# Performance work log

Hardware: AMD Instinct MI355X
Metric: run time of the kernel (lower is better)

Reference implementation:

```python
import jax, jax.numpy as jnp
import numpy as np

N = 50000
E = 800000
IN_DIM = 256
HID = 128
HALF = HID // 2
OUT_DIM = 2


def setup_inputs() -> dict:
    key = jax.random.key(0)
    ks = jax.random.split(key, 16)
    s = lambda fan_in: 1.0 / np.sqrt(fan_in)
    inp = {
        "x": jax.random.normal(ks[0], (N, IN_DIM), dtype=jnp.float32),
        "edge_index": jax.random.randint(ks[1], (2, E), 0, N, dtype=jnp.int64),
        # lin_in: input_dim -> hidden
        "W_in": jax.random.uniform(ks[2], (IN_DIM, HID), jnp.float32, -s(IN_DIM), s(IN_DIM)),
        "b_in": jnp.zeros((HID,), jnp.float32),
        # lin_nor / lin_abnor: half -> hidden
        "W_nor": jax.random.uniform(ks[3], (HALF, HID), jnp.float32, -s(HALF), s(HALF)),
        "b_nor": jnp.zeros((HID,), jnp.float32),
        "W_abnor": jax.random.uniform(ks[4], (HALF, HID), jnp.float32, -s(HALF), s(HALF)),
        "b_abnor": jnp.zeros((HID,), jnp.float32),
        # attention gate
        "W_att": jax.random.uniform(ks[5], (HID, HID), jnp.float32, -s(HID), s(HID)),
        "b_att": jnp.zeros((HID,), jnp.float32),
        "v_att": jax.random.uniform(ks[6], (HID, 1), jnp.float32, -s(HID), s(HID)),
        # update linear
        "W_upd": jax.random.uniform(ks[7], (HID, HID), jnp.float32, -s(HID), s(HID)),
        "b_upd": jnp.zeros((HID,), jnp.float32),
        # classifier
        "W_cls": jax.random.uniform(ks[8], (HID, OUT_DIM), jnp.float32, -s(HID), s(HID)),
        "b_cls": jnp.zeros((OUT_DIM,), jnp.float32),
    }
    return inp


def reference(x, edge_index, W_in, b_in, W_nor, b_nor, W_abnor, b_abnor,
              W_att, b_att, v_att, W_upd, b_upd, W_cls, b_cls):
    n = x.shape[0]
    # add self loops (add_self_loops)
    loops = jnp.tile(jnp.arange(n, dtype=edge_index.dtype), (2, 1))
    ei = jnp.concatenate([edge_index, loops], axis=1)
    row, col = ei[0], ei[1]  # row = source j, col = target i

    # lin_in + leaky_relu (dropout p=0 / eval)
    h = jax.nn.leaky_relu(x @ W_in + b_in)

    # split halves and project
    x_nor = h[:, :HALF] @ W_nor + b_nor      # [N, HID]
    x_abnor = h[:, HALF:] @ W_abnor + b_abnor

    # symmetric normalization by target degree
    deg = jax.ops.segment_sum(jnp.ones_like(col, dtype=h.dtype), col, num_segments=n)
    dinv = jnp.where(deg > 0, jax.lax.rsqrt(jnp.where(deg > 0, deg, 1.0)), 0.0)
    norm = dinv[row] * dinv[col]             # [E']

    # per-edge gather
    xn_j = x_nor[row]                        # [E', HID]
    xa_j = x_abnor[row]

    # denoising attention gate: sigmoid(v^T tanh(W(xn+xa)+b))
    h_att = jnp.tanh((xn_j + xa_j) @ W_att + b_att)
    alpha = jax.nn.sigmoid(h_att @ v_att)    # [E', 1]

    msg = norm[:, None] * (alpha * xn_j + (1.0 - alpha) * xa_j)

    # scatter-add to targets
    aggr = jax.ops.segment_sum(msg, col, num_segments=n)  # [N, HID]

    upd = aggr @ W_upd + b_upd
    out = jax.nn.leaky_relu(upd) @ W_cls + b_cls
    return out
```

## Files before the change

### kernel.cpp

```cpp
#include <hip/hip_runtime.h>

#define N_NODES 50000
#define E_EDGES 800000
#define IN_DIM  256
#define HID     128
#define HALF    64
#define OUT_DIM 2
#define NW      32
#define SLOPE   0.01f

#define ST      132
#define WSLICE  (NW * ST)

#define SSTRIDE 520
#define PLANE   (8 * SSTRIDE)

#define SCAN_B  512
#define SCAN_NB ((N_NODES + SCAN_B - 1) / SCAN_B)

typedef unsigned int uint32;
typedef __attribute__((ext_vector_type(8)))  __bf16 bf16x8v;
typedef __attribute__((ext_vector_type(16))) float  f32x16;

union BF8 { bf16x8v v; unsigned short s[8]; uint4 q; };

#define FI_F 0
#define FN_F 4096
#define FA_F 5120
#define FT_F 6144
#define FU_F 8192
#define F_TOTAL 10240

__device__ __forceinline__ uint32 rne16u(uint32 u) {
    return (u + 0x7fffu + ((u >> 16) & 1u)) >> 16;
}

__device__ __forceinline__ uint32 pack_hl(float v) {
    uint32 uu = __float_as_uint(v);
    uint32 hh = rne16u(uu);
    float  fh = __uint_as_float(hh << 16);
    float  r  = v - fh;
    uint32 ll = rne16u(__float_as_uint(r));
    return (hh << 16) | ll;
}

__device__ __forceinline__ void mfma3(f32x16& acc, bf16x8v ah, bf16x8v al,
                                      bf16x8v bh, bf16x8v bl) {
    acc = __builtin_amdgcn_mfma_f32_32x32x16_bf16(ah, bh, acc, 0, 0, 0);
    acc = __builtin_amdgcn_mfma_f32_32x32x16_bf16(ah, bl, acc, 0, 0, 0);
    acc = __builtin_amdgcn_mfma_f32_32x32x16_bf16(al, bh, acc, 0, 0, 0);
}

__device__ __forceinline__ void stage_split4(__bf16* __restrict__ Ahi,
                                             __bf16* __restrict__ Alo,
                                             int rr, int k, float4 v) {
    int s_idx = k >> 4, jb = k & 7, lt = rr + 32 * ((k >> 3) & 1);
    int base = s_idx * SSTRIDE + lt * 8 + jb;
    float f[4] = {v.x, v.y, v.z, v.w};
    uint32 h[4], lo[4];
    #pragma unroll
    for (int j = 0; j < 4; j++) {
        uint32 uu = __float_as_uint(f[j]);
        uint32 hh = rne16u(uu);
        float  fh = __uint_as_float(hh << 16);
        float  r  = f[j] - fh;
        h[j] = hh; lo[j] = rne16u(__float_as_uint(r));
    }
    *(uint2*)(Ahi + base) = make_uint2(h[0] | (h[1] << 16), h[2] | (h[3] << 16));
    *(uint2*)(Alo + base) = make_uint2(lo[0] | (lo[1] << 16), lo[2] | (lo[3] << 16));
}

__device__ __forceinline__ void mfma_gemm1_pre(f32x16& acc,
        const __bf16* __restrict__ Ahi, const __bf16* __restrict__ Alo,
        int S, int sg0, const uint4* __restrict__ F, int fbase, int l, int t) {
    for (int s = 0; s < S; s++) {
        bf16x8v ah = *(const bf16x8v*)&Ahi[s * SSTRIDE + l * 8];
        bf16x8v al = *(const bf16x8v*)&Alo[s * SSTRIDE + l * 8];
        int f = fbase + ((sg0 + s) * 4 + t) * 64 + l;
        BF8 bh, bl; bh.q = F[2 * f]; bl.q = F[2 * f + 1];
        mfma3(acc, ah, al, bh.v, bl.v);
    }
}

__device__ __forceinline__ void mfma_gemm1_pk(f32x16& acc, const uint32* T,
        int aoff, int S, const uint4* __restrict__ F, int fbase, int l, int t) {
    const int row = l & 31, khi = 8 * (l >> 5);
    for (int s = 0; s < S; s++) {
        int k0 = aoff + 16 * s + khi;
        uint4 qa = *(const uint4*)&T[row * ST + k0];
        uint4 qb = *(const uint4*)&T[row * ST + k0 + 4];
        BF8 ah, al;
        ah.q.x = (qa.x >> 16) | (qa.y & 0xffff0000u);
        ah.q.y = (qa.z >> 16) | (qa.w & 0xffff0000u);
        ah.q.z = (qb.x >> 16) | (qb.y & 0xffff0000u);
        ah.q.w = (qb.z >> 16) | (qb.w & 0xffff0000u);
        al.q.x = (qa.x & 0xffffu) | (qa.y << 16);
        al.q.y = (qa.z & 0xffffu) | (qa.w << 16);
        al.q.z = (qb.x & 0xffffu) | (qb.y << 16);
        al.q.w = (qb.z & 0xffffu) | (qb.w << 16);
        int f = fbase + (s * 4 + t) * 64 + l;
        BF8 bh, bl; bh.q = F[2 * f]; bl.q = F[2 * f + 1];
        mfma3(acc, ah.v, al.v, bh.v, bl.v);
    }
}

__device__ __forceinline__ void mfma_gemm_pre(f32x16* acc,
        const __bf16* __restrict__ Ahi, const __bf16* __restrict__ Alo,
        int S, const uint4* __restrict__ F, int fbase, int l) {
    for (int s = 0; s < S; s++) {
        bf16x8v ah = *(const bf16x8v*)&Ahi[s * SSTRIDE + l * 8];
        bf16x8v al = *(const bf16x8v*)&Alo[s * SSTRIDE + l * 8];
        #pragma unroll
        for (int t = 0; t < 4; t++) {
            int f = fbase + (s * 4 + t) * 64 + l;
            BF8 bh, bl; bh.q = F[2 * f]; bl.q = F[2 * f + 1];
            mfma3(acc[t], ah, al, bh.v, bl.v);
        }
    }
}

__device__ __forceinline__ void initacc(f32x16* acc, const float* __restrict__ b, int col) {
    #pragma unroll
    for (int t = 0; t < 4; t++) {
        float bv = b[32 * t + col];
        #pragma unroll
        for (int r2 = 0; r2 < 16; r2++) acc[t][r2] = bv;
    }
}

__device__ __forceinline__ uint32 pack_bf2(float x, float y) {
    return rne16u(__float_as_uint(x)) | (rne16u(__float_as_uint(y)) << 16);
}

__global__ void zero_int_kernel(int* __restrict__ p, int n) {
    int i = blockIdx.x * blockDim.x + threadIdx.x;
    if (i < n) p[i] = 0;
}

__global__ void deg_ticket_kernel(const int* __restrict__ col,
                                  int* __restrict__ cnt, int* __restrict__ ticket) {
    int e = blockIdx.x * blockDim.x + threadIdx.x;
    if (e < E_EDGES) ticket[e] = atomicAdd(&cnt[col[e]], 1);
}

__device__ __forceinline__ int wave_iscan(int v, int l) {
    #pragma unroll
    for (int off = 1; off < 64; off <<= 1) {
        int t = __shfl_up(v, off, 64);
        if (l >= off) v += t;
    }
    return v;
}

__global__ __launch_bounds__(SCAN_B) void scan1_kernel(
    const int* __restrict__ cnt, int* __restrict__ row_start, int* __restrict__ bsum)
{
    __shared__ int wsum[SCAN_B / 64];
    int i = blockIdx.x * SCAN_B + threadIdx.x;
    int v = (i < N_NODES) ? cnt[i] : 0;
    int l = threadIdx.x & 63, w = threadIdx.x >> 6;
    int isc = wave_iscan(v, l);
    if (l == 63) wsum[w] = isc;
    __syncthreads();
    int wo = 0;
    #pragma unroll
    for (int k = 0; k < SCAN_B / 64; k++) wo += (k < w) ? wsum[k] : 0;
    if (i < N_NODES) row_start[i] = wo + isc - v;
    if (threadIdx.x == SCAN_B - 1) bsum[blockIdx.x] = wo + isc;
}

__global__ __launch_bounds__(128) void scan2_kernel(
    int* __restrict__ bsum, int* __restrict__ row_start)
{
    __shared__ int wsum[2];
    int i = threadIdx.x;
    int v = (i < SCAN_NB) ? bsum[i] : 0;
    int l = i & 63, w = i >> 6;
    int isc = wave_iscan(v, l);
    if (l == 63) wsum[w] = isc;
    __syncthreads();
    int wo = (w == 1) ? wsum[0] : 0;
    if (i < SCAN_NB) bsum[i] = wo + isc - v;
    if (i == SCAN_NB - 1) row_start[N_NODES] = wo + isc;
}

__global__ __launch_bounds__(SCAN_B) void scan3_kernel(
    const int* __restrict__ bsum, int* __restrict__ row_start)
{
    int i = blockIdx.x * SCAN_B + threadIdx.x;
    if (i < N_NODES) row_start[i] += bsum[blockIdx.x];
}

__global__ void fill_kernel(const int* __restrict__ ei,
                            const int* __restrict__ row_start,
                            const int* __restrict__ ticket,
                            int* __restrict__ csr_src)
{
    int e = blockIdx.x * blockDim.x + threadIdx.x;
    if (e >= E_EDGES) return;
    int j = ei[e];
    int i = ei[E_EDGES + e];
    csr_src[row_start[i] + ticket[e]] = j;
}

__global__ __launch_bounds__(256) void prep_w_kernel(
    const float* __restrict__ W_in, const float* __restrict__ W_nor,
    const float* __restrict__ W_ab, const float* __restrict__ W_att,
    const float* __restrict__ W_upd,
    uint4* __restrict__ F)
{
    int idx = blockIdx.x * 256 + threadIdx.x;
    const float* W; int fbase, fi;
    if (idx < 4096)       { W = W_in;  fbase = FI_F; fi = idx; }
    else if (idx < 5120)  { W = W_nor; fbase = FN_F; fi = idx - 4096; }
    else if (idx < 6144)  { W = W_ab;  fbase = FA_F; fi = idx - 5120; }
    else if (idx < 8192)  { W = W_att; fbase = FT_F; fi = idx - 6144; }
    else if (idx < 10240) { W = W_upd; fbase = FU_F; fi = idx - 8192; }
    else return;
    int l = fi & 63, st = fi >> 6, t = st & 3, s = st >> 2;
    int k0 = 16 * s + 8 * (l >> 5);
    int c  = 32 * t + (l & 31);
    uint32 hi[8], lo[8];
    #pragma unroll
    for (int j = 0; j < 8; j++) {
        float v = W[(size_t)(k0 + j) * HID + c];
        uint32 uu = __float_as_uint(v);
        uint32 h  = rne16u(uu);
        float  fh = __uint_as_float(h << 16);
        float  r  = v - fh;
        hi[j] = h;
        lo[j] = rne16u(__float_as_uint(r));
    }
    uint4 H, L;
    H.x = hi[0] | (hi[1] << 16); H.y = hi[2] | (hi[3] << 16);
    H.z = hi[4] | (hi[5] << 16); H.w = hi[6] | (hi[7] << 16);
    L.x = lo[0] | (lo[1] << 16); L.y = lo[2] | (lo[3] << 16);
    L.z = lo[4] | (lo[5] << 16); L.w = lo[6] | (lo[7] << 16);
    int f = fbase + fi;
    F[2 * f]     = H;
    F[2 * f + 1] = L;
}

__global__ __launch_bounds__(256, 4) void node_phase_kernel(
    const float* __restrict__ x,
    const float* __restrict__ b_in,  const float* __restrict__ b_nor,
    const float* __restrict__ b_abnor, const float* __restrict__ b_att,
    const float* __restrict__ v_att,
    const int* __restrict__ cnt,
    const uint4* __restrict__ F,
    uint32* __restrict__ u)
{
    __shared__ __align__(16) float smem[WSLICE];
    __shared__ float dinvs[NW];
    __shared__ float gpart[4][NW];
    __bf16* Ahi = (__bf16*)smem;
    __bf16* Alo = (__bf16*)smem + PLANE;
    uint32* T   = (uint32*)smem;

    const int tid    = threadIdx.x;
    const int w      = tid >> 6;
    const int l      = tid & 63;
    const int col    = l & 31;
    const int hi     = l >> 5;
    const int wnode0 = blockIdx.x * NW;

    if (tid < NW) {
        int nd = wnode0 + tid;
        float c = (nd < N_NODES) ? (float)cnt[nd] : 0.f;
        dinvs[tid] = rsqrtf(c + 1.0f);
    }

    f32x16 hacc;
    {
        float bv = b_in[32 * w + col];
        #pragma unroll
        for (int r2 = 0; r2 < 16; r2++) hacc[r2] = bv;
    }
    for (int half = 0; half < 2; half++) {
        #pragma unroll
        for (int it = 0; it < 4; it++) {
            int i = it * 256 + tid;
            int rr = i >> 5, kq = i & 31, k = 4 * kq;
            int nd = wnode0 + rr; if (nd >= N_NODES) nd = N_NODES - 1;
            float4 v = *(const float4*)(x + (size_t)nd * IN_DIM + half * 128 + k);
            stage_split4(Ahi, Alo, rr, k, v);
        }
        __syncthreads();
        mfma_gemm1_pre(hacc, Ahi, Alo, 8, half * 8, F, FI_F, l, w);
        __syncthreads();
    }

    #pragma unroll
    for (int rg = 0; rg < 16; rg++) {
        int rrow = (rg & 3) + 8 * (rg >> 2) + 4 * hi;
        float v = hacc[rg];
        v = v > 0.f ? v : SLOPE * v;
        T[rrow * ST + 32 * w + col] = pack_hl(v);
    }
    __syncthreads();

    f32x16 xn, xa;
    {
        float bv = b_nor[32 * w + col];
        #pragma unroll
        for (int r2 = 0; r2 < 16; r2++) xn[r2] = bv;
    }
    mfma_gemm1_pk(xn, T, 0, 4, F, FN_F, l, w);
    {
        float bv = b_abnor[32 * w + col];
        #pragma unroll
        for (int r2 = 0; r2 < 16; r2++) xa[r2] = bv;
    }
    mfma_gemm1_pk(xa, T, HALF, 4, F, FA_F, l, w);
    __syncthreads();

    f32x16 sv, d;
    #pragma unroll
    for (int rg = 0; rg < 16; rg++) {
        int rrow = (rg & 3) + 8 * (rg >> 2) + 4 * hi;
        sv[rg] = xn[rg] + xa[rg];
        d[rg]  = xn[rg] - xa[rg];
        T[rrow * ST + 32 * w + col] = pack_hl(sv[rg]);
    }
    __syncthreads();

    f32x16 tac;
    {
        float bv = b_att[32 * w + col];
        #pragma unroll
        for (int r2 = 0; r2 < 16; r2++) tac[r2] = bv;
    }
    mfma_gemm1_pk(tac, T, 0, 8, F, FT_F, l, w);

    float g[16];
    {
        float vv = v_att[32 * w + col];
        #pragma unroll
        for (int rg = 0; rg < 16; rg++) g[rg] = tanhf(tac[rg]) * vv;
    }
    #pragma unroll
    for (int msk = 16; msk >= 1; msk >>= 1) {
        #pragma unroll
        for (int rg = 0; rg < 16; rg++) g[rg] += __shfl_xor(g[rg], msk, 64);
    }
    if (col == 0) {
        #pragma unroll
        for (int rg = 0; rg < 16; rg++) {
            int rrow = (rg & 3) + 8 * (rg >> 2) + 4 * hi;
            gpart[w][rrow] = g[rg];
        }
    }
    __syncthreads();

    float am[16];
    #pragma unroll
    for (int rg = 0; rg < 16; rg++) {
        int rrow = (rg & 3) + 8 * (rg >> 2) + 4 * hi;
        float gt = gpart[0][rrow] + gpart[1][rrow] + gpart[2][rrow] + gpart[3][rrow];
        am[rg] = 1.f / (1.f + expf(-gt)) - 0.5f;
    }

    #pragma unroll
    for (int rg = 0; rg < 16; rg++) {
        int rrow = (rg & 3) + 8 * (rg >> 2) + 4 * hi;
        int n    = wnode0 + rrow;
        float uv = dinvs[rrow] * (0.5f * sv[rg] + am[rg] * d[rg]);
        float pv = __shfl_xor(uv, 1, 64);
        if (((l & 1) == 0) && n < N_NODES) {
            u[(size_t)n * (HID / 2) + 16 * w + (col >> 1)] = pack_bf2(uv, pv);
        }
    }
}

__global__ __launch_bounds__(256) void gather_kernel(
    const int* __restrict__ row_start, const int* __restrict__ csr_src,
    const uint32* __restrict__ u, float* __restrict__ acc)
{
    int node = blockIdx.x * 4 + (threadIdx.x >> 6);
    int lane = threadIdx.x & 63;
    if (node >= N_NODES) return;

    const size_t RW = HID / 2;
    uint32 v = u[(size_t)node * RW + lane];
    float sx = __uint_as_float(v << 16);
    float sy = __uint_as_float(v & 0xffff0000u);

    int b = row_start[node], e = row_start[node + 1];
    int p = b;
    for (; p + 8 <= e; p += 8) {
        int j0 = csr_src[p + 0], j1 = csr_src[p + 1];
        int j2 = csr_src[p + 2], j3 = csr_src[p + 3];
        int j4 = csr_src[p + 4], j5 = csr_src[p + 5];
        int j6 = csr_src[p + 6], j7 = csr_src[p + 7];
        uint32 v0 = u[(size_t)j0 * RW + lane];
        uint32 v1 = u[(size_t)j1 * RW + lane];
        uint32 v2 = u[(size_t)j2 * RW + lane];
        uint32 v3 = u[(size_t)j3 * RW + lane];
        uint32 v4 = u[(size_t)j4 * RW + lane];
        uint32 v5 = u[(size_t)j5 * RW + lane];
        uint32 v6 = u[(size_t)j6 * RW + lane];
        uint32 v7 = u[(size_t)j7 * RW + lane];
        sx += __uint_as_float(v0 << 16) + __uint_as_float(v1 << 16)
            + __uint_as_float(v2 << 16) + __uint_as_float(v3 << 16)
            + __uint_as_float(v4 << 16) + __uint_as_float(v5 << 16)
            + __uint_as_float(v6 << 16) + __uint_as_float(v7 << 16);
        sy += __uint_as_float(v0 & 0xffff0000u) + __uint_as_float(v1 & 0xffff0000u)
            + __uint_as_float(v2 & 0xffff0000u) + __uint_as_float(v3 & 0xffff0000u)
            + __uint_as_float(v4 & 0xffff0000u) + __uint_as_float(v5 & 0xffff0000u)
            + __uint_as_float(v6 & 0xffff0000u) + __uint_as_float(v7 & 0xffff0000u);
    }
    for (; p < e; p++) {
        int j = csr_src[p];
        uint32 w = u[(size_t)j * RW + lane];
        sx += __uint_as_float(w << 16);
        sy += __uint_as_float(w & 0xffff0000u);
    }
    float2 s = make_float2(sx, sy);
    *(float2*)(acc + (size_t)node * HID + lane * 2) = s;
}

__global__ __launch_bounds__(64, 2) void final_phase_kernel(
    const float* __restrict__ acc, const int* __restrict__ cnt,
    const float* __restrict__ b_upd,
    const float* __restrict__ W_cls, const float* __restrict__ b_cls,
    const uint4* __restrict__ F,
    float* __restrict__ out)
{
    __shared__ __align__(16) float smem[WSLICE];
    __bf16* Ahi = (__bf16*)smem;
    __bf16* Alo = (__bf16*)smem + PLANE;

    const int l      = threadIdx.x;
    const int col    = l & 31;
    const int wnode0 = blockIdx.x * NW;

    #pragma unroll
    for (int it = 0; it < 16; it++) {
        int i = it * 64 + l;
        int rr = i >> 5, kq = i & 31, k = 4 * kq;
        int nd = wnode0 + rr; if (nd >= N_NODES) nd = N_NODES - 1;
        float dv = rsqrtf((float)cnt[nd] + 1.0f);
        float4 v = *(const float4*)(acc + (size_t)nd * HID + k);
        v.x *= dv; v.y *= dv; v.z *= dv; v.w *= dv;
        stage_split4(Ahi, Alo, rr, k, v);
    }

    f32x16 up[4];
    initacc(up, b_upd, col);
    mfma_gemm_pre(up, Ahi, Alo, 8, F, FU_F, l);

    float* B = smem;
    #pragma unroll
    for (int t = 0; t < 4; t++) {
        #pragma unroll
        for (int rg = 0; rg < 16; rg++) {
            int rrow = (rg & 3) + 8 * (rg >> 2) + 4 * (l >> 5);
            float v = up[t][rg];
            B[rrow * ST + 32 * t + col] = v > 0.f ? v : SLOPE * v;
        }
    }

    {
        int n = l >> 1, o = l & 1;
        if (wnode0 + n < N_NODES) {
            float s = b_cls[o];
            for (int k = 0; k < HID; k++)
                s = fmaf(B[n * ST + k], W_cls[k * OUT_DIM + o], s);
            out[(size_t)(wnode0 + n) * OUT_DIM + o] = s;
        }
    }
}

extern "C" void kernel_launch(void* const* d_in, const int* in_sizes, int n_in,
                              void* d_out, int out_size, void* d_ws, size_t ws_size,
                              hipStream_t stream)
{
    const float* x       = (const float*)d_in[0];
    const int*   ei      = (const int*)  d_in[1];
    const float* W_in    = (const float*)d_in[2];
    const float* b_in    = (const float*)d_in[3];
    const float* W_nor   = (const float*)d_in[4];
    const float* b_nor   = (const float*)d_in[5];
    const float* W_abnor = (const float*)d_in[6];
    const float* b_abnor = (const float*)d_in[7];
    const float* W_att   = (const float*)d_in[8];
    const float* b_att   = (const float*)d_in[9];
    const float* v_att   = (const float*)d_in[10];
    const float* W_upd   = (const float*)d_in[11];
    const float* b_upd   = (const float*)d_in[12];
    const float* W_cls   = (const float*)d_in[13];
    const float* b_cls   = (const float*)d_in[14];
    float* out = (float*)d_out;

    char* base = (char*)d_ws;
    int*  cnt       = (int*)base;
    int*  row_start = cnt + N_NODES;
    int*  bsum      = row_start + (N_NODES + 1);
    int*  csr_src   = bsum + 128;
    size_t off_u    = (((size_t)(2 * N_NODES + 129 + E_EDGES)) * 4 + 63) & ~(size_t)63;
    uint32* u       = (uint32*)(base + off_u);
    size_t off_acc  = (off_u + (size_t)N_NODES * (HID / 2) * 4 + 63) & ~(size_t)63;
    float* acc      = (float*)(base + off_acc);
    int*   ticket   = (int*)acc;
    size_t off_f    = (off_acc + (size_t)N_NODES * HID * 4 + 63) & ~(size_t)63;
    uint4* F        = (uint4*)(base + off_f);

    const int nblk = (N_NODES + NW - 1) / NW;

    zero_int_kernel<<<(N_NODES + 255) / 256, 256, 0, stream>>>(cnt, N_NODES);
    deg_ticket_kernel<<<(E_EDGES + 255) / 256, 256, 0, stream>>>(ei + E_EDGES, cnt, ticket);
    scan1_kernel<<<SCAN_NB, SCAN_B, 0, stream>>>(cnt, row_start, bsum);
    scan2_kernel<<<1, 128, 0, stream>>>(bsum, row_start);
    scan3_kernel<<<SCAN_NB, SCAN_B, 0, stream>>>(bsum, row_start);
    fill_kernel<<<(E_EDGES + 255) / 256, 256, 0, stream>>>(ei, row_start, ticket, csr_src);
    prep_w_kernel<<<F_TOTAL / 256, 256, 0, stream>>>(W_in, W_nor, W_abnor, W_att, W_upd, F);
    node_phase_kernel<<<nblk, 256, 0, stream>>>(
        x, b_in, b_nor, b_abnor, b_att, v_att, cnt, F, u);
    gather_kernel<<<(N_NODES + 3) / 4, 256, 0, stream>>>(row_start, csr_src, u, acc);
    final_phase_kernel<<<nblk, 64, 0, stream>>>(
        acc, cnt, b_upd, W_cls, b_cls, F, out);
}
```

Before: 165.0 us.

## Use fast tanh/sigmoid, masked 8-wide gather loop, 4-wave final phase

Swaps tanhf and expf-based sigmoid for exp plus hardware reciprocal approximations in the attention gate. The gather loop is restructured so every iteration issues 8 clamped index loads and 8 row loads, with masking instead of a scalar tail, to keep more loads in flight for low-degree nodes. The final phase moves from one wave to four waves per block, with each wave computing one 32-column slice of the update GEMM and the classifier dot product split across 4 lanes per output and combined by shuffle reduction. The approximate transcendentals change numerics slightly, and the masked tail issues redundant loads.

```diff
diff --git a/kernel.cpp b/kernel.cpp
--- a/kernel.cpp
+++ b/kernel.cpp
@@ -42,6 +42,14 @@
     float  r  = v - fh;
     uint32 ll = rne16u(__float_as_uint(r));
     return (hh << 16) | ll;
+}
+
+__device__ __forceinline__ float fast_tanh(float x) {
+    float ex = __expf(2.f * x);
+    return 1.f - 2.f * __builtin_amdgcn_rcpf(ex + 1.f);
+}
+__device__ __forceinline__ float fast_sig(float x) {
+    return __builtin_amdgcn_rcpf(1.f + __expf(-x));
 }
 
 __device__ __forceinline__ void mfma3(f32x16& acc, bf16x8v ah, bf16x8v al,
@@ -104,30 +112,6 @@
     }
 }
 
-__device__ __forceinline__ void mfma_gemm_pre(f32x16* acc,
-        const __bf16* __restrict__ Ahi, const __bf16* __restrict__ Alo,
-        int S, const uint4* __restrict__ F, int fbase, int l) {
-    for (int s = 0; s < S; s++) {
-        bf16x8v ah = *(const bf16x8v*)&Ahi[s * SSTRIDE + l * 8];
-        bf16x8v al = *(const bf16x8v*)&Alo[s * SSTRIDE + l * 8];
-        #pragma unroll
-        for (int t = 0; t < 4; t++) {
-            int f = fbase + (s * 4 + t) * 64 + l;
-            BF8 bh, bl; bh.q = F[2 * f]; bl.q = F[2 * f + 1];
-            mfma3(acc[t], ah, al, bh.v, bl.v);
-        }
-    }
-}
-
-__device__ __forceinline__ void initacc(f32x16* acc, const float* __restrict__ b, int col) {
-    #pragma unroll
-    for (int t = 0; t < 4; t++) {
-        float bv = b[32 * t + col];
-        #pragma unroll
-        for (int r2 = 0; r2 < 16; r2++) acc[t][r2] = bv;
-    }
-}
-
 __device__ __forceinline__ uint32 pack_bf2(float x, float y) {
     return rne16u(__float_as_uint(x)) | (rne16u(__float_as_uint(y)) << 16);
 }
@@ -336,7 +320,7 @@
     {
         float vv = v_att[32 * w + col];
         #pragma unroll
-        for (int rg = 0; rg < 16; rg++) g[rg] = tanhf(tac[rg]) * vv;
+        for (int rg = 0; rg < 16; rg++) g[rg] = fast_tanh(tac[rg]) * vv;
     }
     #pragma unroll
     for (int msk = 16; msk >= 1; msk >>= 1) {
@@ -357,7 +341,7 @@
     for (int rg = 0; rg < 16; rg++) {
         int rrow = (rg & 3) + 8 * (rg >> 2) + 4 * hi;
         float gt = gpart[0][rrow] + gpart[1][rrow] + gpart[2][rrow] + gpart[3][rrow];
-        am[rg] = 1.f / (1.f + expf(-gt)) - 0.5f;
+        am[rg] = fast_sig(gt) - 0.5f;
     }
 
     #pragma unroll
@@ -386,40 +370,29 @@
     float sy = __uint_as_float(v & 0xffff0000u);
 
     int b = row_start[node], e = row_start[node + 1];
-    int p = b;
-    for (; p + 8 <= e; p += 8) {
-        int j0 = csr_src[p + 0], j1 = csr_src[p + 1];
-        int j2 = csr_src[p + 2], j3 = csr_src[p + 3];
-        int j4 = csr_src[p + 4], j5 = csr_src[p + 5];
-        int j6 = csr_src[p + 6], j7 = csr_src[p + 7];
-        uint32 v0 = u[(size_t)j0 * RW + lane];
-        uint32 v1 = u[(size_t)j1 * RW + lane];
-        uint32 v2 = u[(size_t)j2 * RW + lane];
-        uint32 v3 = u[(size_t)j3 * RW + lane];
-        uint32 v4 = u[(size_t)j4 * RW + lane];
-        uint32 v5 = u[(size_t)j5 * RW + lane];
-        uint32 v6 = u[(size_t)j6 * RW + lane];
-        uint32 v7 = u[(size_t)j7 * RW + lane];
-        sx += __uint_as_float(v0 << 16) + __uint_as_float(v1 << 16)
-            + __uint_as_float(v2 << 16) + __uint_as_float(v3 << 16)
-            + __uint_as_float(v4 << 16) + __uint_as_float(v5 << 16)
-            + __uint_as_float(v6 << 16) + __uint_as_float(v7 << 16);
-        sy += __uint_as_float(v0 & 0xffff0000u) + __uint_as_float(v1 & 0xffff0000u)
-            + __uint_as_float(v2 & 0xffff0000u) + __uint_as_float(v3 & 0xffff0000u)
-            + __uint_as_float(v4 & 0xffff0000u) + __uint_as_float(v5 & 0xffff0000u)
-            + __uint_as_float(v6 & 0xffff0000u) + __uint_as_float(v7 & 0xffff0000u);
-    }
-    for (; p < e; p++) {
-        int j = csr_src[p];
-        uint32 w = u[(size_t)j * RW + lane];
-        sx += __uint_as_float(w << 16);
-        sy += __uint_as_float(w & 0xffff0000u);
+    for (int p = b; p < e; p += 8) {
+        int idx[8];
+        #pragma unroll
+        for (int q = 0; q < 8; q++) {
+            int a = p + q; if (a > e - 1) a = e - 1;
+            idx[q] = csr_src[a];
+        }
+        uint32 vv[8];
+        #pragma unroll
+        for (int q = 0; q < 8; q++) vv[q] = u[(size_t)idx[q] * RW + lane];
+        #pragma unroll
+        for (int q = 0; q < 8; q++) {
+            if (p + q < e) {
+                sx += __uint_as_float(vv[q] << 16);
+                sy += __uint_as_float(vv[q] & 0xffff0000u);
+            }
+        }
     }
     float2 s = make_float2(sx, sy);
     *(float2*)(acc + (size_t)node * HID + lane * 2) = s;
 }
 
-__global__ __launch_bounds__(64, 2) void final_phase_kernel(
+__global__ __launch_bounds__(256, 4) void final_phase_kernel(
     const float* __restrict__ acc, const int* __restrict__ cnt,
     const float* __restrict__ b_upd,
     const float* __restrict__ W_cls, const float* __restrict__ b_cls,
@@ -430,13 +403,16 @@
     __bf16* Ahi = (__bf16*)smem;
     __bf16* Alo = (__bf16*)smem + PLANE;
 
-    const int l      = threadIdx.x;
+    const int tid    = threadIdx.x;
+    const int w      = tid >> 6;
+    const int l      = tid & 63;
     const int col    = l & 31;
+    const int hi     = l >> 5;
     const int wnode0 = blockIdx.x * NW;
 
     #pragma unroll
-    for (int it = 0; it < 16; it++) {
-        int i = it * 64 + l;
+    for (int it = 0; it < 4; it++) {
+        int i = it * 256 + tid;
         int rr = i >> 5, kq = i & 31, k = 4 * kq;
         int nd = wnode0 + rr; if (nd >= N_NODES) nd = N_NODES - 1;
         float dv = rsqrtf((float)cnt[nd] + 1.0f);
@@ -444,29 +420,36 @@
         v.x *= dv; v.y *= dv; v.z *= dv; v.w *= dv;
         stage_split4(Ahi, Alo, rr, k, v);
     }
-
-    f32x16 up[4];
-    initacc(up, b_upd, col);
-    mfma_gemm_pre(up, Ahi, Alo, 8, F, FU_F, l);
+    __syncthreads();
+
+    f32x16 up;
+    {
+        float bv = b_upd[32 * w + col];
+        #pragma unroll
+        for (int r2 = 0; r2 < 16; r2++) up[r2] = bv;
+    }
+    mfma_gemm1_pre(up, Ahi, Alo, 8, 0, F, FU_F, l, w);
+    __syncthreads();
 
     float* B = smem;
     #pragma unroll
-    for (int t = 0; t < 4; t++) {
-        #pragma unroll
-        for (int rg = 0; rg < 16; rg++) {
-            int rrow = (rg & 3) + 8 * (rg >> 2) + 4 * (l >> 5);
-            float v = up[t][rg];
-            B[rrow * ST + 32 * t + col] = v > 0.f ? v : SLOPE * v;
-        }
-    }
-
-    {
-        int n = l >> 1, o = l & 1;
-        if (wnode0 + n < N_NODES) {
-            float s = b_cls[o];
-            for (int k = 0; k < HID; k++)
-                s = fmaf(B[n * ST + k], W_cls[k * OUT_DIM + o], s);
-            out[(size_t)(wnode0 + n) * OUT_DIM + o] = s;
+    for (int rg = 0; rg < 16; rg++) {
+        int rrow = (rg & 3) + 8 * (rg >> 2) + 4 * hi;
+        float v = up[rg];
+        B[rrow * ST + 32 * w + col] = v > 0.f ? v : SLOPE * v;
+    }
+    __syncthreads();
+
+    {
+        int n = tid >> 3, o = (tid >> 2) & 1, c = tid & 3;
+        float s = 0.f;
+        int k0 = c * 32;
+        for (int k = k0; k < k0 + 32; k++)
+            s = fmaf(B[n * ST + k], W_cls[k * OUT_DIM + o], s);
+        s += __shfl_xor(s, 1, 64);
+        s += __shfl_xor(s, 2, 64);
+        if (c == 0 && wnode0 + n < N_NODES) {
+            out[(size_t)(wnode0 + n) * OUT_DIM + o] = s + b_cls[o];
         }
     }
 }
@@ -517,6 +500,6 @@
     node_phase_kernel<<<nblk, 256, 0, stream>>>(
         x, b_in, b_nor, b_abnor, b_att, v_att, cnt, F, u);
     gather_kernel<<<(N_NODES + 3) / 4, 256, 0, stream>>>(row_start, csr_src, u, acc);
-    final_phase_kernel<<<nblk, 64, 0, stream>>>(
+    final_phase_kernel<<<nblk, 256, 0, stream>>>(
         acc, cnt, b_upd, W_cls, b_cls, F, out);
 }
```

Result: no change. 162.0 us (-1.8%).
